# Kernel tuning notes

Hardware: AMD Instinct MI355X
Metric: run time of the kernel (lower is better)

## Reference

```python
import jax, jax.numpy as jnp
import numpy as np

NEG_SLOPE = 0.2  # PyG GATv2Conv default negative_slope


def gatv2_conv(x, src, dst, Wl, Wr, att, bias, concat):
    # x: [N, Fin]; src/dst: [E]; Wl/Wr: [Fin, H*C]; att: [H, C]
    N = x.shape[0]
    H, C = att.shape
    xl = (x @ Wl).reshape(N, H, C)
    xr = (x @ Wr).reshape(N, H, C)
    m = jax.nn.leaky_relu(xl[src] + xr[dst], NEG_SLOPE)          # [E,H,C]
    logits = jnp.einsum('ehc,hc->eh', m, att)                    # [E,H]
    lmax = jax.ops.segment_max(logits, dst, num_segments=N)      # stable softmax per dst segment
    ex = jnp.exp(logits - lmax[dst])
    denom = jax.ops.segment_sum(ex, dst, num_segments=N)
    alpha = ex / (denom[dst] + 1e-16)
    out = jax.ops.segment_sum(xl[src] * alpha[:, :, None], dst, num_segments=N)  # [N,H,C]
    out = out.reshape(N, H * C) if concat else out.mean(axis=1)
    return out + bias


def setup_inputs() -> dict:
    key = jax.random.key(0)
    ks = jax.random.split(key, 9)
    bsz, T, n_nodes = 8, 100, 2048
    Cin, hid, H, Cout = 128, 64, 4, 128
    inp = jax.random.normal(ks[0], (bsz, T, n_nodes), jnp.float32)
    ei = jax.random.randint(ks[1], (2, 32768), 0, n_nodes, jnp.int32)
    # remove self loops (PyG remove_self_loops before adding them back)
    ei = ei.at[1].set(jnp.where(ei[0] == ei[1], (ei[1] + 1) % n_nodes, ei[1]))

    def lin(k, fi, fo):
        return jax.random.normal(k, (fi, fo), jnp.float32) / np.sqrt(fi).astype(np.float32)

    return {
        'input': inp, 'edge_index': ei,
        'W_temb': lin(ks[2], T, Cin), 'b_temb': jnp.zeros((Cin,), jnp.float32),
        'Wl1': lin(ks[3], Cin, H * hid), 'Wr1': lin(ks[4], Cin, H * hid),
        'att1': jax.random.normal(ks[5], (H, hid), jnp.float32) / np.sqrt(hid).astype(np.float32),
        'b1': jnp.zeros((H * hid,), jnp.float32),
        'Wl2': lin(ks[6], H * hid, Cout), 'Wr2': lin(ks[7], H * hid, Cout),
        'att2': jax.random.normal(ks[8], (1, Cout), jnp.float32) / np.sqrt(Cout).astype(np.float32),
        'b2': jnp.zeros((Cout,), jnp.float32),
    }


def reference(input, edge_index, W_temb, b_temb, Wl1, Wr1, att1, b1, Wl2, Wr2, att2, b2):
    bsz, T, n_nodes = input.shape
    N = bsz * n_nodes
    # temporal embedding: [B,T,n] -> [B,n,T] @ [T,Cin] -> flatten to [N,Cin]
    x = (jnp.swapaxes(input, 1, 2) @ W_temb + b_temb).reshape(N, -1)
    # faithful to source: edge_index.repeat(1, bsz) tiles edges with NO batch offset;
    # GATv2Conv then adds self loops over all N nodes
    loops = jnp.arange(N, dtype=edge_index.dtype)
    src = jnp.concatenate([jnp.tile(edge_index[0], bsz), loops])
    dst = jnp.concatenate([jnp.tile(edge_index[1], bsz), loops])
    x = gatv2_conv(x, src, dst, Wl1, Wr1, att1, b1, True)
    x = jax.nn.elu(x)
    x = gatv2_conv(x, src, dst, Wl2, Wr2, att2, b2, False)
    return x.reshape(bsz, n_nodes, -1).mean(axis=1)  # [bsz, out_channels]
```

## Files before the change

kernel.cpp:

```cpp
#include <hip/hip_runtime.h>
#include <hip/hip_bf16.h>
#include <math.h>

#define NEG_SLOPE 0.2f

constexpr int BSZ = 8, T = 100, NN = 2048, N = BSZ * NN;
constexpr int CIN = 128, F1 = 256, F2 = 128;
constexpr int E = 32768;
constexpr int KP = 40;
constexpr int MAXDEG = 64;

typedef _Float16 f16x8 __attribute__((ext_vector_type(8)));
typedef float f32x4 __attribute__((ext_vector_type(4)));

__device__ inline float lrelu(float m) { return m > 0.f ? m : NEG_SLOPE * m; }
__device__ inline float eluf(float v) { return v > 0.f ? v : expm1f(v); }

__global__ __launch_bounds__(256) void k_prep_cvt(const float* __restrict__ in,
        const float* __restrict__ Wt,
        const float* __restrict__ Wl1, const float* __restrict__ Wr1,
        const float* __restrict__ Wl2, const float* __restrict__ Wr2,
        const float* __restrict__ b2,
        _Float16* __restrict__ Tt, _Float16* __restrict__ T1l,
        _Float16* __restrict__ T1r, _Float16* __restrict__ T2l,
        _Float16* __restrict__ T2r, int* __restrict__ cnt, float* __restrict__ out,
        _Float16* __restrict__ xTh) {
    __shared__ __align__(16) char smem[26016];
    const int job = blockIdx.x;
    const int t = threadIdx.x;
    if (job < 145) {
        if (job == 144) {
            for (int i = t; i < NN; i += 256) cnt[i] = 0;
            for (int i = t; i < BSZ * F2; i += 256) out[i] = b2[i & (F2 - 1)];
            return;
        }
        int which, base;
        if (job < 16)       { which = 0; base = 0; }
        else if (job < 48)  { which = 1; base = 16; }
        else if (job < 80)  { which = 2; base = 48; }
        else if (job < 112) { which = 3; base = 80; }
        else                { which = 4; base = 112; }
        const int Ks[5] = {100, 128, 128, 256, 256};
        const int Kd[5] = {128, 128, 128, 256, 256};
        const int Nc[5] = {128, 256, 256, 128, 128};
        const float* Wsrc[5] = {Wt, Wl1, Wr1, Wl2, Wr2};
        _Float16* Wdst[5] = {Tt, T1l, T1r, T2l, T2r};
        int rel = job - base;
        int ks = Ks[which], kd = Kd[which], nc = Nc[which];
        int tilesN = nc / 32;
        int tk = (rel / tilesN) * 32, tn = (rel % tilesN) * 32;
        const float* src = Wsrc[which];
        _Float16* dst = Wdst[which];
        _Float16 (*tile)[33] = (_Float16(*)[33])smem;
        int tx = t & 31, ty = t >> 5;
        for (int r = ty; r < 32; r += 8)
            tile[r][tx] = (tk + r < ks) ? (_Float16)src[(tk + r) * nc + tn + tx] : (_Float16)0.f;
        __syncthreads();
        for (int r = ty; r < 32; r += 8)
            dst[(tn + r) * kd + tk + tx] = tile[tx][r];
        return;
    }
    float* lt = (float*)smem;
    const int blk = job - 145;
    const int b = blk >> 5, node0 = (blk & 31) * 64;
    for (int i = t; i < T * 64; i += 256) {
        int tt = i >> 6, n = i & 63;
        lt[tt * 65 + n] = in[(b * T + tt) * NN + node0 + n];
    }
    __syncthreads();
    const int node = t >> 2, seg = t & 3;
    _Float16* dst = &xTh[(size_t)(b * NN + node0 + node) * 128 + seg * 32];
    #pragma unroll
    for (int j = 0; j < 4; ++j) {
        f16x8 v;
        #pragma unroll
        for (int e = 0; e < 8; ++e) {
            int k = seg * 32 + j * 8 + e;
            v[e] = (k < T) ? (_Float16)lt[k * 65 + node] : (_Float16)0.f;
        }
        *(f16x8*)&dst[j * 8] = v;
    }
}

__global__ __launch_bounds__(512) void k_gm1f_scat(const _Float16* __restrict__ xTh,
        const _Float16* __restrict__ Tt, const float* __restrict__ bt,
        const _Float16* __restrict__ T1l, const _Float16* __restrict__ T1r,
        const float* __restrict__ b1, const int* __restrict__ ei,
        int* __restrict__ cnt, int* __restrict__ srcs,
        float* __restrict__ xl1, float* __restrict__ xr1, _Float16* __restrict__ h1h) {
    const int t = threadIdx.x;
    if (blockIdx.x >= 512) {
        int i = (blockIdx.x - 512) * 512 + t;
        int d = ei[E + i];
        int slot = atomicAdd(&cnt[d], 1);
        if (slot < MAXDEG) srcs[d * MAXDEG + slot] = ei[i];
        return;
    }
    __shared__ __align__(16) char smem[8704 + 40960];
    _Float16* xt  = (_Float16*)smem;
    _Float16* stg = (_Float16*)(smem + 8704);
    const int wave = t >> 6, lane = t & 63;
    const int quad = lane >> 4, l15 = lane & 15;
    const int row0 = blockIdx.x * 32;
    #pragma unroll
    for (int it = 0; it < 4; ++it) {
        int idx = t + it * 512;
        int col = idx >> 4, j = idx & 15;
        *(f16x8*)&stg[col * 136 + j * 8] = *(const f16x8*)&Tt[col * 128 + j * 8];
    }
    __syncthreads();
    {
        const int wcol = wave * 16 + l15;
        f32x4 a0 = {0,0,0,0}, a1 = {0,0,0,0};
        #pragma unroll
        for (int kt = 0; kt < 128; kt += 32) {
            f16x8 af0 = *(const f16x8*)&xTh[(size_t)(row0 + l15) * 128 + kt + quad * 8];
            f16x8 af1 = *(const f16x8*)&xTh[(size_t)(row0 + 16 + l15) * 128 + kt + quad * 8];
            f16x8 bf  = *(const f16x8*)&stg[wcol * 136 + kt + quad * 8];
            a0 = __builtin_amdgcn_mfma_f32_16x16x32_f16(af0, bf, a0, 0, 0, 0);
            a1 = __builtin_amdgcn_mfma_f32_16x16x32_f16(af1, bf, a1, 0, 0, 0);
        }
        float bv = bt[wcol];
        #pragma unroll
        for (int r = 0; r < 4; ++r) {
            xt[(quad * 4 + r) * 136 + wcol]      = (_Float16)(a0[r] + bv);
            xt[(16 + quad * 4 + r) * 136 + wcol] = (_Float16)(a1[r] + bv);
        }
    }
    __syncthreads();
    const int mat = wave >> 2, cg4 = wave & 3;
    const int nmats = (row0 < NN) ? 2 : 1;
    f32x4 acc[2][4];
    #pragma unroll
    for (int s = 0; s < 2; ++s)
        #pragma unroll
        for (int c = 0; c < 4; ++c) acc[s][c] = (f32x4){0,0,0,0};
    for (int kt = 0; kt < CIN; kt += 32) {
        if (kt) __syncthreads();
        for (int it = 0; it < nmats * 2; ++it) {
            int idx = t + it * 512;
            int m = idx >> 10, rem = idx & 1023;
            int col = rem >> 2, j = rem & 3;
            const _Float16* src = (m ? T1r : T1l) + col * CIN + kt + j * 8;
            *(f16x8*)&stg[(m * 256 + col) * KP + j * 8] = *(const f16x8*)src;
        }
        __syncthreads();
        f16x8 af0 = *(const f16x8*)&xt[l15 * 136 + kt + quad * 8];
        f16x8 af1 = *(const f16x8*)&xt[(16 + l15) * 136 + kt + quad * 8];
        if (mat < nmats) {
            #pragma unroll
            for (int ct = 0; ct < 4; ++ct) {
                int col = cg4 * 64 + ct * 16 + l15;
                f16x8 bf = *(const f16x8*)&stg[(mat * 256 + col) * KP + quad * 8];
                acc[0][ct] = __builtin_amdgcn_mfma_f32_16x16x32_f16(af0, bf, acc[0][ct], 0, 0, 0);
                acc[1][ct] = __builtin_amdgcn_mfma_f32_16x16x32_f16(af1, bf, acc[1][ct], 0, 0, 0);
            }
        }
    }
    if (row0 < NN) {
        float* dst = mat ? xr1 : xl1;
        #pragma unroll
        for (int s = 0; s < 2; ++s)
            #pragma unroll
            for (int ct = 0; ct < 4; ++ct) {
                int col = cg4 * 64 + ct * 16 + l15;
                #pragma unroll
                for (int r = 0; r < 4; ++r)
                    dst[(row0 + s * 16 + quad * 4 + r) * F1 + col] = acc[s][ct][r];
            }
    } else if (mat == 0) {
        #pragma unroll
        for (int ct = 0; ct < 4; ++ct) {
            int col = cg4 * 64 + ct * 16 + l15;
            float bv = b1[col];
            #pragma unroll
            for (int s = 0; s < 2; ++s)
                #pragma unroll
                for (int r = 0; r < 4; ++r)
                    h1h[(size_t)(row0 + s * 16 + quad * 4 + r) * F1 + col] =
                        (_Float16)eluf(acc[s][ct][r] + bv);
        }
    }
}

__global__ __launch_bounds__(256) void k_gat1_gm2s(const int* __restrict__ cnt,
        const int* __restrict__ srcs, const float* __restrict__ xl1,
        const float* __restrict__ xr1, const float* __restrict__ att1,
        const float* __restrict__ b1, _Float16* __restrict__ h1h,
        const _Float16* __restrict__ T2l, float* __restrict__ out) {
    __shared__ __align__(16) char smem[10304];
    const int t = threadIdx.x;
    const int wave = t >> 6, lane = t & 63;
    if (blockIdx.x >= 2048) {
        _Float16* bs = (_Float16*)smem;
        const int quad = lane >> 4, l15 = lane & 15;
        const int row0 = NN + (blockIdx.x - 2048) * 32;
        f32x4 acc[2][2];
        #pragma unroll
        for (int s = 0; s < 2; ++s)
            #pragma unroll
            for (int c = 0; c < 2; ++c) acc[s][c] = (f32x4){0,0,0,0};
        for (int kt = 0; kt < F1; kt += 32) {
            if (kt) __syncthreads();
            #pragma unroll
            for (int it = 0; it < 2; ++it) {
                int idx = t + it * 256;
                int col = idx >> 2, j = idx & 3;
                *(f16x8*)&bs[col * KP + j * 8] = *(const f16x8*)&T2l[col * F1 + kt + j * 8];
            }
            __syncthreads();
            f16x8 af0 = *(const f16x8*)&h1h[(size_t)(row0 + l15) * F1 + kt + quad * 8];
            f16x8 af1 = *(const f16x8*)&h1h[(size_t)(row0 + 16 + l15) * F1 + kt + quad * 8];
            #pragma unroll
            for (int ct = 0; ct < 2; ++ct) {
                int col = wave * 32 + ct * 16 + l15;
                f16x8 bf = *(const f16x8*)&bs[col * KP + quad * 8];
                acc[0][ct] = __builtin_amdgcn_mfma_f32_16x16x32_f16(af0, bf, acc[0][ct], 0, 0, 0);
                acc[1][ct] = __builtin_amdgcn_mfma_f32_16x16x32_f16(af1, bf, acc[1][ct], 0, 0, 0);
            }
        }
        int b = row0 >> 11;
        #pragma unroll
        for (int ct = 0; ct < 2; ++ct) {
            float s8 = 0.f;
            #pragma unroll
            for (int s = 0; s < 2; ++s)
                #pragma unroll
                for (int r = 0; r < 4; ++r) s8 += acc[s][ct][r];
            s8 += __shfl_xor(s8, 16, 64);
            s8 += __shfl_xor(s8, 32, 64);
            if (quad == 0)
                atomicAdd(&out[b * F2 + wave * 32 + ct * 16 + l15], s8 * (1.0f / NN));
        }
        return;
    }
    const int d = blockIdx.x;
    const int wv = wave, c = lane;
    int deg = cnt[d]; deg = deg < MAXDEG ? deg : MAXDEG;
    float b[4], at[4], sh[4], acc[4] = {0,0,0,0}, dnl[4] = {0,0,0,0};
    #pragma unroll
    for (int k = 0; k < 4; ++k) {
        b[k]  = xr1[d * F1 + c + 64 * k];
        at[k] = att1[c + 64 * k];
        sh[k] = lrelu(xl1[d * F1 + c + 64 * k] + b[k]) * at[k];
    }
    #pragma unroll
    for (int o = 32; o; o >>= 1) {
        #pragma unroll
        for (int k = 0; k < 4; ++k) sh[k] += __shfl_xor(sh[k], o, 64);
    }
    for (int e = wv; e < deg; e += 4) {
        int s = srcs[d * MAXDEG + e];
        float a[4], p[4];
        #pragma unroll
        for (int k = 0; k < 4; ++k) {
            a[k] = xl1[s * F1 + c + 64 * k];
            p[k] = lrelu(a[k] + b[k]) * at[k];
        }
        #pragma unroll
        for (int o = 32; o; o >>= 1) {
            #pragma unroll
            for (int k = 0; k < 4; ++k) p[k] += __shfl_xor(p[k], o, 64);
        }
        #pragma unroll
        for (int k = 0; k < 4; ++k) {
            float w = 8.0f * __expf(p[k] - sh[k]);
            dnl[k] += w;
            acc[k] = fmaf(w, a[k], acc[k]);
        }
    }
    float (*lacc)[F1] = (float(*)[F1])smem;
    float (*ldn)[4]   = (float(*)[4])(smem + 4096);
    #pragma unroll
    for (int k = 0; k < 4; ++k) lacc[wv][c + 64 * k] = acc[k];
    if (c < 4) ldn[wv][c] = dnl[c];
    __syncthreads();
    int f = t, h = t >> 6;
    float tot = xl1[d * F1 + f] + lacc[0][f] + lacc[1][f] + lacc[2][f] + lacc[3][f];
    float dnf = 1.0f + ldn[0][h] + ldn[1][h] + ldn[2][h] + ldn[3][h];
    h1h[(size_t)d * F1 + f] = (_Float16)eluf(tot / (dnf + 1e-16f) + b1[f]);
}

__global__ __launch_bounds__(512) void k_gm2loc(const _Float16* __restrict__ h1h,
        const _Float16* __restrict__ T2l, const _Float16* __restrict__ T2r,
        float* __restrict__ xl2, float* __restrict__ xr2) {
    __shared__ __align__(16) _Float16 bs[2 * 128 * KP];
    const int t = threadIdx.x;
    const int wave = t >> 6, lane = t & 63;
    const int quad = lane >> 4, l15 = lane & 15;
    const int mat = wave >> 2, cg4 = wave & 3;
    const int row0 = blockIdx.x * 32;
    f32x4 acc[2][2];
    #pragma unroll
    for (int s = 0; s < 2; ++s)
        #pragma unroll
        for (int c = 0; c < 2; ++c) acc[s][c] = (f32x4){0,0,0,0};
    for (int kt = 0; kt < F1; kt += 32) {
        if (kt) __syncthreads();
        #pragma unroll
        for (int it = 0; it < 2; ++it) {
            int idx = t + it * 512;
            int m = idx >> 9, rem = idx & 511;
            int col = rem >> 2, j = rem & 3;
            const _Float16* src = (m ? T2r : T2l) + col * F1 + kt + j * 8;
            *(f16x8*)&bs[(m * 128 + col) * KP + j * 8] = *(const f16x8*)src;
        }
        __syncthreads();
        f16x8 af0 = *(const f16x8*)&h1h[(size_t)(row0 + l15) * F1 + kt + quad * 8];
        f16x8 af1 = *(const f16x8*)&h1h[(size_t)(row0 + 16 + l15) * F1 + kt + quad * 8];
        #pragma unroll
        for (int ct = 0; ct < 2; ++ct) {
            int col = cg4 * 32 + ct * 16 + l15;
            f16x8 bf = *(const f16x8*)&bs[(mat * 128 + col) * KP + quad * 8];
            acc[0][ct] = __builtin_amdgcn_mfma_f32_16x16x32_f16(af0, bf, acc[0][ct], 0, 0, 0);
            acc[1][ct] = __builtin_amdgcn_mfma_f32_16x16x32_f16(af1, bf, acc[1][ct], 0, 0, 0);
        }
    }
    float* dst = mat ? xr2 : xl2;
    #pragma unroll
    for (int s = 0; s < 2; ++s)
        #pragma unroll
        for (int ct = 0; ct < 2; ++ct) {
            int col = cg4 * 32 + ct * 16 + l15;
            #pragma unroll
            for (int r = 0; r < 4; ++r)
                dst[(row0 + s * 16 + quad * 4 + r) * F2 + col] = acc[s][ct][r];
        }
}

__global__ __launch_bounds__(256) void k_gat2(const int* __restrict__ cnt,
        const int* __restrict__ srcs, const float* __restrict__ xl2,
        const float* __restrict__ xr2, const float* __restrict__ att2,
        float* __restrict__ acc2) {
    const int d = blockIdx.x;
    const int t = threadIdx.x;
    const int wv = t >> 6, c = t & 63;
    int deg = cnt[d]; deg = deg < MAXDEG ? deg : MAXDEG;
    float b0 = xr2[d * F2 + c], b1v = xr2[d * F2 + c + 64];
    float at0 = att2[c], at1 = att2[c + 64];
    float sh = lrelu(xl2[d * F2 + c] + b0) * at0 + lrelu(xl2[d * F2 + c + 64] + b1v) * at1;
    #pragma unroll
    for (int o = 32; o; o >>= 1) sh += __shfl_xor(sh, o, 64);
    float acc0 = 0.f, acc1v = 0.f, dnl = 0.f;
    for (int e = wv; e < deg; e += 4) {
        int s = srcs[d * MAXDEG + e];
        float a0 = xl2[s * F2 + c], a1 = xl2[s * F2 + c + 64];
        float p = lrelu(a0 + b0) * at0 + lrelu(a1 + b1v) * at1;
        #pragma unroll
        for (int o = 32; o; o >>= 1) p += __shfl_xor(p, o, 64);
        float w = 8.0f * __expf(p - sh);
        dnl += w;
        acc0 = fmaf(w, a0, acc0);
        acc1v = fmaf(w, a1, acc1v);
    }
    __shared__ float lacc[4][F2];
    __shared__ float ldn[4];
    lacc[wv][c] = acc0;
    lacc[wv][c + 64] = acc1v;
    if (c == 0) ldn[wv] = dnl;
    __syncthreads();
    if (t < F2) {
        int f = t;
        float dnf = 1.0f + ldn[0] + ldn[1] + ldn[2] + ldn[3] + 1e-16f;
        acc2[d * F2 + f] =
            (xl2[d * F2 + f] + lacc[0][f] + lacc[1][f] + lacc[2][f] + lacc[3][f]) / dnf;
    }
}

__global__ __launch_bounds__(128) void k_out0(const float* __restrict__ acc2,
        float* __restrict__ out) {
    int chunk = blockIdx.x;
    int c = threadIdx.x;
    float s = 0.f;
    int n0 = chunk * 64;
    for (int i = 0; i < 64; ++i)
        s += acc2[(n0 + i) * F2 + c];
    atomicAdd(&out[c], s * (1.0f / NN));
}

extern "C" void kernel_launch(void* const* d_in, const int* in_sizes, int n_in,
                              void* d_out, int out_size, void* d_ws, size_t ws_size,
                              hipStream_t stream) {
    const float* in   = (const float*)d_in[0];
    const int*   ei   = (const int*)d_in[1];
    const float* Wt   = (const float*)d_in[2];
    const float* bt   = (const float*)d_in[3];
    const float* Wl1  = (const float*)d_in[4];
    const float* Wr1  = (const float*)d_in[5];
    const float* att1 = (const float*)d_in[6];
    const float* b1   = (const float*)d_in[7];
    const float* Wl2  = (const float*)d_in[8];
    const float* Wr2  = (const float*)d_in[9];
    const float* att2 = (const float*)d_in[10];
    const float* b2   = (const float*)d_in[11];
    float* out = (float*)d_out;

    float* ws = (float*)d_ws;
    _Float16* xTh = (_Float16*)ws;
    _Float16* h1h = xTh + (size_t)N * 128;
    float* xl1  = (float*)(h1h + (size_t)N * F1);
    float* xr1  = xl1 + NN * F1;
    float* xl2  = xr1 + NN * F1;
    float* xr2  = xl2 + NN * F2;
    float* acc2 = xr2 + NN * F2;
    _Float16* Tt  = (_Float16*)(acc2 + NN * F2);
    _Float16* T1l = Tt + 128 * 128;
    _Float16* T1r = T1l + 256 * 128;
    _Float16* T2l = T1r + 256 * 128;
    _Float16* T2r = T2l + 128 * 256;
    int* cnt  = (int*)(T2r + 128 * 256);
    int* srcs = cnt + NN;

    k_prep_cvt<<<401, 256, 0, stream>>>(in, Wt, Wl1, Wr1, Wl2, Wr2, b2,
                                        Tt, T1l, T1r, T2l, T2r, cnt, out, xTh);
    k_gm1f_scat<<<576, 512, 0, stream>>>(xTh, Tt, bt, T1l, T1r, b1, ei, cnt, srcs,
                                         xl1, xr1, h1h);
    k_gat1_gm2s<<<2496, 256, 0, stream>>>(cnt, srcs, xl1, xr1, att1, b1, h1h, T2l, out);
    k_gm2loc<<<64, 512, 0, stream>>>(h1h, T2l, T2r, xl2, xr2);
    k_gat2<<<NN, 256, 0, stream>>>(cnt, srcs, xl2, xr2, att2, acc2);
    k_out0<<<32, 128, 0, stream>>>(acc2, out);
}
```

Measured before the change: 138.4 us.

## Fuse input transpose and second-layer self-loop GEMM into first GEMM kernel

The separate fp16 transpose of the input into a workspace buffer is removed. k_gm1 now loads and converts its 32-row tile of raw input directly into shared memory. For the self-loop-only rows (batches 1..7), the ELU output stays in shared memory and the second-layer GEMM plus mean reduction into out is done in the same block, so h1h is no longer written and re-read for those rows. This saves global traffic and shrinks the gat1 grid, at the cost of more shared memory per block and strided uncoalesced input reads.

```diff
diff --git a/kernel.cpp b/kernel.cpp
--- a/kernel.cpp
+++ b/kernel.cpp
@@ -16,78 +16,53 @@
 __device__ inline float lrelu(float m) { return m > 0.f ? m : NEG_SLOPE * m; }
 __device__ inline float eluf(float v) { return v > 0.f ? v : expm1f(v); }
 
-__global__ __launch_bounds__(256) void k_prep_cvt(const float* __restrict__ in,
-        const float* __restrict__ Wt,
+__global__ __launch_bounds__(256) void k_prep(const float* __restrict__ Wt,
         const float* __restrict__ Wl1, const float* __restrict__ Wr1,
         const float* __restrict__ Wl2, const float* __restrict__ Wr2,
         const float* __restrict__ b2,
         _Float16* __restrict__ Tt, _Float16* __restrict__ T1l,
         _Float16* __restrict__ T1r, _Float16* __restrict__ T2l,
-        _Float16* __restrict__ T2r, int* __restrict__ cnt, float* __restrict__ out,
-        _Float16* __restrict__ xTh) {
-    __shared__ __align__(16) char smem[26016];
+        _Float16* __restrict__ T2r, int* __restrict__ cnt, float* __restrict__ out) {
+    __shared__ _Float16 tile[32][33];
     const int job = blockIdx.x;
     const int t = threadIdx.x;
-    if (job < 145) {
-        if (job == 144) {
-            for (int i = t; i < NN; i += 256) cnt[i] = 0;
-            for (int i = t; i < BSZ * F2; i += 256) out[i] = b2[i & (F2 - 1)];
-            return;
-        }
-        int which, base;
-        if (job < 16)       { which = 0; base = 0; }
-        else if (job < 48)  { which = 1; base = 16; }
-        else if (job < 80)  { which = 2; base = 48; }
-        else if (job < 112) { which = 3; base = 80; }
-        else                { which = 4; base = 112; }
-        const int Ks[5] = {100, 128, 128, 256, 256};
-        const int Kd[5] = {128, 128, 128, 256, 256};
-        const int Nc[5] = {128, 256, 256, 128, 128};
-        const float* Wsrc[5] = {Wt, Wl1, Wr1, Wl2, Wr2};
-        _Float16* Wdst[5] = {Tt, T1l, T1r, T2l, T2r};
-        int rel = job - base;
-        int ks = Ks[which], kd = Kd[which], nc = Nc[which];
-        int tilesN = nc / 32;
-        int tk = (rel / tilesN) * 32, tn = (rel % tilesN) * 32;
-        const float* src = Wsrc[which];
-        _Float16* dst = Wdst[which];
-        _Float16 (*tile)[33] = (_Float16(*)[33])smem;
-        int tx = t & 31, ty = t >> 5;
-        for (int r = ty; r < 32; r += 8)
-            tile[r][tx] = (tk + r < ks) ? (_Float16)src[(tk + r) * nc + tn + tx] : (_Float16)0.f;
-        __syncthreads();
-        for (int r = ty; r < 32; r += 8)
-            dst[(tn + r) * kd + tk + tx] = tile[tx][r];
+    if (job == 144) {
+        for (int i = t; i < NN; i += 256) cnt[i] = 0;
+        for (int i = t; i < BSZ * F2; i += 256) out[i] = b2[i & (F2 - 1)];
         return;
     }
-    float* lt = (float*)smem;
-    const int blk = job - 145;
-    const int b = blk >> 5, node0 = (blk & 31) * 64;
-    for (int i = t; i < T * 64; i += 256) {
-        int tt = i >> 6, n = i & 63;
-        lt[tt * 65 + n] = in[(b * T + tt) * NN + node0 + n];
-    }
-    __syncthreads();
-    const int node = t >> 2, seg = t & 3;
-    _Float16* dst = &xTh[(size_t)(b * NN + node0 + node) * 128 + seg * 32];
-    #pragma unroll
-    for (int j = 0; j < 4; ++j) {
-        f16x8 v;
-        #pragma unroll
-        for (int e = 0; e < 8; ++e) {
-            int k = seg * 32 + j * 8 + e;
-            v[e] = (k < T) ? (_Float16)lt[k * 65 + node] : (_Float16)0.f;
-        }
-        *(f16x8*)&dst[j * 8] = v;
-    }
-}
-
-__global__ __launch_bounds__(512) void k_gm1f_scat(const _Float16* __restrict__ xTh,
+    int which, base;
+    if (job < 16)       { which = 0; base = 0; }
+    else if (job < 48)  { which = 1; base = 16; }
+    else if (job < 80)  { which = 2; base = 48; }
+    else if (job < 112) { which = 3; base = 80; }
+    else                { which = 4; base = 112; }
+    const int Ks[5] = {100, 128, 128, 256, 256};
+    const int Kd[5] = {128, 128, 128, 256, 256};
+    const int Nc[5] = {128, 256, 256, 128, 128};
+    const float* Wsrc[5] = {Wt, Wl1, Wr1, Wl2, Wr2};
+    _Float16* Wdst[5] = {Tt, T1l, T1r, T2l, T2r};
+    int rel = job - base;
+    int ks = Ks[which], kd = Kd[which], nc = Nc[which];
+    int tilesN = nc / 32;
+    int tk = (rel / tilesN) * 32, tn = (rel % tilesN) * 32;
+    const float* src = Wsrc[which];
+    _Float16* dst = Wdst[which];
+    int tx = t & 31, ty = t >> 5;
+    for (int r = ty; r < 32; r += 8)
+        tile[r][tx] = (tk + r < ks) ? (_Float16)src[(tk + r) * nc + tn + tx] : (_Float16)0.f;
+    __syncthreads();
+    for (int r = ty; r < 32; r += 8)
+        dst[(tn + r) * kd + tk + tx] = tile[tx][r];
+}
+
+__global__ __launch_bounds__(512) void k_gm1(const float* __restrict__ in,
         const _Float16* __restrict__ Tt, const float* __restrict__ bt,
         const _Float16* __restrict__ T1l, const _Float16* __restrict__ T1r,
-        const float* __restrict__ b1, const int* __restrict__ ei,
-        int* __restrict__ cnt, int* __restrict__ srcs,
-        float* __restrict__ xl1, float* __restrict__ xr1, _Float16* __restrict__ h1h) {
+        const float* __restrict__ b1, const _Float16* __restrict__ T2l,
+        const int* __restrict__ ei, int* __restrict__ cnt, int* __restrict__ srcs,
+        float* __restrict__ xl1, float* __restrict__ xr1,
+        _Float16* __restrict__ h1h, float* __restrict__ out) {
     const int t = threadIdx.x;
     if (blockIdx.x >= 512) {
         int i = (blockIdx.x - 512) * 512 + t;
@@ -96,17 +71,30 @@
         if (slot < MAXDEG) srcs[d * MAXDEG + slot] = ei[i];
         return;
     }
-    __shared__ __align__(16) char smem[8704 + 40960];
-    _Float16* xt  = (_Float16*)smem;
-    _Float16* stg = (_Float16*)(smem + 8704);
+    __shared__ __align__(16) char smem[8704 + 43520];
+    _Float16* xt = (_Float16*)smem;
+    char* sh = smem + 8704;
     const int wave = t >> 6, lane = t & 63;
     const int quad = lane >> 4, l15 = lane & 15;
+    const int mat = wave >> 2, cg4 = wave & 3;
     const int row0 = blockIdx.x * 32;
+    _Float16* stgT = (_Float16*)sh;
+    _Float16* inA  = (_Float16*)(sh + 34816);
     #pragma unroll
     for (int it = 0; it < 4; ++it) {
         int idx = t + it * 512;
         int col = idx >> 4, j = idx & 15;
-        *(f16x8*)&stg[col * 136 + j * 8] = *(const f16x8*)&Tt[col * 128 + j * 8];
+        *(f16x8*)&stgT[col * 136 + j * 8] = *(const f16x8*)&Tt[col * 128 + j * 8];
+    }
+    {
+        const int b = row0 >> 11, node0 = row0 & (NN - 1);
+        const float* ip = in + (size_t)b * T * NN + node0;
+        #pragma unroll
+        for (int it = 0; it < 8; ++it) {
+            int idx = t + it * 512;
+            int tt = idx >> 5, n = idx & 31;
+            inA[n * 136 + tt] = (tt < T) ? (_Float16)ip[tt * NN + n] : (_Float16)0.f;
+        }
     }
     __syncthreads();
     {
@@ -114,9 +102,9 @@
         f32x4 a0 = {0,0,0,0}, a1 = {0,0,0,0};
         #pragma unroll
         for (int kt = 0; kt < 128; kt += 32) {
-            f16x8 af0 = *(const f16x8*)&xTh[(size_t)(row0 + l15) * 128 + kt + quad * 8];
-            f16x8 af1 = *(const f16x8*)&xTh[(size_t)(row0 + 16 + l15) * 128 + kt + quad * 8];
-            f16x8 bf  = *(const f16x8*)&stg[wcol * 136 + kt + quad * 8];
+            f16x8 af0 = *(const f16x8*)&inA[l15 * 136 + kt + quad * 8];
+            f16x8 af1 = *(const f16x8*)&inA[(16 + l15) * 136 + kt + quad * 8];
+            f16x8 bf  = *(const f16x8*)&stgT[wcol * 136 + kt + quad * 8];
             a0 = __builtin_amdgcn_mfma_f32_16x16x32_f16(af0, bf, a0, 0, 0, 0);
             a1 = __builtin_amdgcn_mfma_f32_16x16x32_f16(af1, bf, a1, 0, 0, 0);
         }
@@ -128,7 +116,7 @@
         }
     }
     __syncthreads();
-    const int mat = wave >> 2, cg4 = wave & 3;
+    _Float16* stg = (_Float16*)sh;
     const int nmats = (row0 < NN) ? 2 : 1;
     f32x4 acc[2][4];
     #pragma unroll
@@ -168,7 +156,12 @@
                 for (int r = 0; r < 4; ++r)
                     dst[(row0 + s * 16 + quad * 4 + r) * F1 + col] = acc[s][ct][r];
             }
-    } else if (mat == 0) {
+        return;
+    }
+    __syncthreads();
+    _Float16* stg2 = (_Float16*)sh;
+    _Float16* hrow = (_Float16*)(sh + 10240);
+    if (mat == 0) {
         #pragma unroll
         for (int ct = 0; ct < 4; ++ct) {
             int col = cg4 * 64 + ct * 16 + l15;
@@ -177,65 +170,42 @@
             for (int s = 0; s < 2; ++s)
                 #pragma unroll
                 for (int r = 0; r < 4; ++r)
-                    h1h[(size_t)(row0 + s * 16 + quad * 4 + r) * F1 + col] =
+                    hrow[(s * 16 + quad * 4 + r) * 264 + col] =
                         (_Float16)eluf(acc[s][ct][r] + bv);
         }
     }
-}
-
-__global__ __launch_bounds__(256) void k_gat1_gm2s(const int* __restrict__ cnt,
+    __syncthreads();
+    f32x4 c0 = {0,0,0,0}, c1 = {0,0,0,0};
+    const int colw = wave * 16 + l15;
+    for (int kt = 0; kt < F1; kt += 32) {
+        if (kt) __syncthreads();
+        {
+            int col = t >> 2, j = t & 3;
+            *(f16x8*)&stg2[col * KP + j * 8] = *(const f16x8*)&T2l[col * F1 + kt + j * 8];
+        }
+        __syncthreads();
+        f16x8 a0 = *(const f16x8*)&hrow[l15 * 264 + kt + quad * 8];
+        f16x8 a1 = *(const f16x8*)&hrow[(16 + l15) * 264 + kt + quad * 8];
+        f16x8 bf = *(const f16x8*)&stg2[colw * KP + quad * 8];
+        c0 = __builtin_amdgcn_mfma_f32_16x16x32_f16(a0, bf, c0, 0, 0, 0);
+        c1 = __builtin_amdgcn_mfma_f32_16x16x32_f16(a1, bf, c1, 0, 0, 0);
+    }
+    float s8 = c0[0] + c0[1] + c0[2] + c0[3] + c1[0] + c1[1] + c1[2] + c1[3];
+    s8 += __shfl_xor(s8, 16, 64);
+    s8 += __shfl_xor(s8, 32, 64);
+    if (quad == 0)
+        atomicAdd(&out[(row0 >> 11) * F2 + colw], s8 * (1.0f / NN));
+}
+
+__global__ __launch_bounds__(256) void k_gat1(const int* __restrict__ cnt,
         const int* __restrict__ srcs, const float* __restrict__ xl1,
         const float* __restrict__ xr1, const float* __restrict__ att1,
-        const float* __restrict__ b1, _Float16* __restrict__ h1h,
-        const _Float16* __restrict__ T2l, float* __restrict__ out) {
-    __shared__ __align__(16) char smem[10304];
-    const int t = threadIdx.x;
-    const int wave = t >> 6, lane = t & 63;
-    if (blockIdx.x >= 2048) {
-        _Float16* bs = (_Float16*)smem;
-        const int quad = lane >> 4, l15 = lane & 15;
-        const int row0 = NN + (blockIdx.x - 2048) * 32;
-        f32x4 acc[2][2];
-        #pragma unroll
-        for (int s = 0; s < 2; ++s)
-            #pragma unroll
-            for (int c = 0; c < 2; ++c) acc[s][c] = (f32x4){0,0,0,0};
-        for (int kt = 0; kt < F1; kt += 32) {
-            if (kt) __syncthreads();
-            #pragma unroll
-            for (int it = 0; it < 2; ++it) {
-                int idx = t + it * 256;
-                int col = idx >> 2, j = idx & 3;
-                *(f16x8*)&bs[col * KP + j * 8] = *(const f16x8*)&T2l[col * F1 + kt + j * 8];
-            }
-            __syncthreads();
-            f16x8 af0 = *(const f16x8*)&h1h[(size_t)(row0 + l15) * F1 + kt + quad * 8];
-            f16x8 af1 = *(const f16x8*)&h1h[(size_t)(row0 + 16 + l15) * F1 + kt + quad * 8];
-            #pragma unroll
-            for (int ct = 0; ct < 2; ++ct) {
-                int col = wave * 32 + ct * 16 + l15;
-                f16x8 bf = *(const f16x8*)&bs[col * KP + quad * 8];
-                acc[0][ct] = __builtin_amdgcn_mfma_f32_16x16x32_f16(af0, bf, acc[0][ct], 0, 0, 0);
-                acc[1][ct] = __builtin_amdgcn_mfma_f32_16x16x32_f16(af1, bf, acc[1][ct], 0, 0, 0);
-            }
-        }
-        int b = row0 >> 11;
-        #pragma unroll
-        for (int ct = 0; ct < 2; ++ct) {
-            float s8 = 0.f;
-            #pragma unroll
-            for (int s = 0; s < 2; ++s)
-                #pragma unroll
-                for (int r = 0; r < 4; ++r) s8 += acc[s][ct][r];
-            s8 += __shfl_xor(s8, 16, 64);
-            s8 += __shfl_xor(s8, 32, 64);
-            if (quad == 0)
-                atomicAdd(&out[b * F2 + wave * 32 + ct * 16 + l15], s8 * (1.0f / NN));
-        }
-        return;
-    }
+        const float* __restrict__ b1, _Float16* __restrict__ h1h) {
+    __shared__ float lacc[4][F1];
+    __shared__ float ldn[4][4];
+    const int t = threadIdx.x;
+    const int wv = t >> 6, c = t & 63;
     const int d = blockIdx.x;
-    const int wv = wave, c = lane;
     int deg = cnt[d]; deg = deg < MAXDEG ? deg : MAXDEG;
     float b[4], at[4], sh[4], acc[4] = {0,0,0,0}, dnl[4] = {0,0,0,0};
     #pragma unroll
@@ -269,8 +239,6 @@
             acc[k] = fmaf(w, a[k], acc[k]);
         }
     }
-    float (*lacc)[F1] = (float(*)[F1])smem;
-    float (*ldn)[4]   = (float(*)[4])(smem + 4096);
     #pragma unroll
     for (int k = 0; k < 4; ++k) lacc[wv][c + 64 * k] = acc[k];
     if (c < 4) ldn[wv][c] = dnl[c];
@@ -373,6 +341,7 @@
     int c = threadIdx.x;
     float s = 0.f;
     int n0 = chunk * 64;
+    #pragma unroll 8
     for (int i = 0; i < 64; ++i)
         s += acc2[(n0 + i) * F2 + c];
     atomicAdd(&out[c], s * (1.0f / NN));
@@ -396,9 +365,8 @@
     float* out = (float*)d_out;
 
     float* ws = (float*)d_ws;
-    _Float16* xTh = (_Float16*)ws;
-    _Float16* h1h = xTh + (size_t)N * 128;
-    float* xl1  = (float*)(h1h + (size_t)N * F1);
+    _Float16* h1h = (_Float16*)ws;
+    float* xl1  = (float*)(h1h + (size_t)NN * F1);
     float* xr1  = xl1 + NN * F1;
     float* xl2  = xr1 + NN * F1;
     float* xr2  = xl2 + NN * F2;
@@ -411,11 +379,11 @@
     int* cnt  = (int*)(T2r + 128 * 256);
     int* srcs = cnt + NN;
 
-    k_prep_cvt<<<401, 256, 0, stream>>>(in, Wt, Wl1, Wr1, Wl2, Wr2, b2,
-                                        Tt, T1l, T1r, T2l, T2r, cnt, out, xTh);
-    k_gm1f_scat<<<576, 512, 0, stream>>>(xTh, Tt, bt, T1l, T1r, b1, ei, cnt, srcs,
-                                         xl1, xr1, h1h);
-    k_gat1_gm2s<<<2496, 256, 0, stream>>>(cnt, srcs, xl1, xr1, att1, b1, h1h, T2l, out);
+    k_prep<<<145, 256, 0, stream>>>(Wt, Wl1, Wr1, Wl2, Wr2, b2,
+                                    Tt, T1l, T1r, T2l, T2r, cnt, out);
+    k_gm1<<<576, 512, 0, stream>>>(in, Tt, bt, T1l, T1r, b1, T2l, ei, cnt, srcs,
+                                   xl1, xr1, h1h, out);
+    k_gat1<<<2048, 256, 0, stream>>>(cnt, srcs, xl1, xr1, att1, b1, h1h);
     k_gm2loc<<<64, 512, 0, stream>>>(h1h, T2l, T2r, xl2, xr2);
     k_gat2<<<NN, 256, 0, stream>>>(cnt, srcs, xl2, xr2, att2, acc2);
     k_out0<<<32, 128, 0, stream>>>(acc2, out);
```

Measured after the change: 134.2 us. 3.1% less time.
